# Kernel optimization log

Measured on AMD Instinct MI355X. Metric: run time of the kernel, lower is better.

Reference implementation:

```python
import jax, jax.numpy as jnp
import numpy as np

# Architecture constants (from init_kwargs)
IN_DIM, D_MODEL, HEADDIM, D_STATE, EXPAND, OUT_DIM = 57, 64, 32, 32, 2, 6
D_INNER = EXPAND * D_MODEL          # 128
NHEADS = D_INNER // HEADDIM         # 4
D_CONV = 4                          # causal depthwise conv width (mamba default)
D_XBC = D_INNER + 2 * D_STATE       # 192 (x, B, C share the conv)
D_IN_PROJ = 2 * D_INNER + 2 * D_STATE + NHEADS  # z, xBC, dt -> 324
BATCH, SEQ = 16, 2048


def setup_inputs() -> dict:
    key = jax.random.key(0)
    ks = jax.random.split(key, 12)
    s = 0.02
    return {
        "x": jax.random.normal(ks[0], (BATCH, SEQ, IN_DIM), jnp.float32),
        "W_lin": jax.random.normal(ks[1], (IN_DIM, D_MODEL), jnp.float32) * s,
        "b_lin": jnp.zeros((D_MODEL,), jnp.float32),
        "W_in": jax.random.normal(ks[2], (D_MODEL, D_IN_PROJ), jnp.float32) * s,
        "conv_w": jax.random.normal(ks[3], (D_XBC, 1, D_CONV), jnp.float32) * 0.5,
        "conv_b": jnp.zeros((D_XBC,), jnp.float32),
        "dt_bias": jnp.log(jax.random.uniform(ks[4], (NHEADS,), jnp.float32, 0.001, 0.1)),
        "A_log": jnp.log(jnp.arange(1, NHEADS + 1, dtype=jnp.float32)),
        "D": jnp.ones((NHEADS,), jnp.float32),
        "norm_w": jnp.ones((D_INNER,), jnp.float32),
        "W_out": jax.random.normal(ks[5], (D_INNER, D_MODEL), jnp.float32) * s,
        "W_cls": jax.random.normal(ks[6], (D_MODEL, OUT_DIM), jnp.float32) * s,
        "b_cls": jnp.zeros((OUT_DIM,), jnp.float32),
    }


def _mamba_block(h, W_in, conv_w, conv_b, dt_bias, A_log, D, norm_w, W_out):
    B, L, _ = h.shape
    zxbcdt = h @ W_in                                   # [B,L,324]
    z = zxbcdt[..., :D_INNER]                           # gate [B,L,128]
    xBC = zxbcdt[..., D_INNER:D_INNER + D_XBC]          # [B,L,192]
    dt = zxbcdt[..., D_INNER + D_XBC:]                  # [B,L,H]

    # causal depthwise conv over time + silu
    xBC = jax.lax.conv_general_dilated(
        xBC.transpose(0, 2, 1), conv_w, (1,), [(D_CONV - 1, 0)],
        dimension_numbers=("NCH", "OIH", "NCH"), feature_group_count=D_XBC)
    xBC = jax.nn.silu(xBC + conv_b[None, :, None]).transpose(0, 2, 1)

    xs = xBC[..., :D_INNER].reshape(B, L, NHEADS, HEADDIM)   # [B,L,H,P]
    Bm = xBC[..., D_INNER:D_INNER + D_STATE]                 # [B,L,N]
    Cm = xBC[..., D_INNER + D_STATE:]                        # [B,L,N]

    dt = jax.nn.softplus(dt + dt_bias)                       # [B,L,H]
    A = -jnp.exp(A_log)                                      # [H]

    def step(hstate, t):
        dtt, xt, bt, ct = t                                  # [B,H],[B,H,P],[B,N],[B,N]
        decay = jnp.exp(dtt * A)[:, :, None, None]           # [B,H,1,1]
        hstate = hstate * decay + (dtt[:, :, None] * xt)[..., None] * bt[:, None, None, :]
        y = jnp.einsum("bhpn,bn->bhp", hstate, ct)
        return hstate, y

    h0 = jnp.zeros((B, NHEADS, HEADDIM, D_STATE), h.dtype)
    _, ys = jax.lax.scan(step, h0, (dt.transpose(1, 0, 2), xs.transpose(1, 0, 2, 3),
                                    Bm.transpose(1, 0, 2), Cm.transpose(1, 0, 2)))
    y = ys.transpose(1, 0, 2, 3) + D[None, None, :, None] * xs   # [B,L,H,P]
    y = y.reshape(B, L, D_INNER)

    # gated RMSNorm + out proj
    y = y * jax.nn.silu(z)
    y = y * jax.lax.rsqrt(jnp.mean(y * y, axis=-1, keepdims=True) + 1e-5) * norm_w
    return y @ W_out                                        # [B,L,D_MODEL]


def reference(x, W_lin, b_lin, W_in, conv_w, conv_b, dt_bias, A_log, D, norm_w,
              W_out, W_cls, b_cls):
    h = x @ W_lin + b_lin                                   # linear_in
    h = _mamba_block(h, W_in, conv_w, conv_b, dt_bias, A_log, D, norm_w, W_out)
    pooled = h.mean(axis=1)                                 # AdaptiveAvgPool1d(1)
    return pooled @ W_cls + b_cls                           # classifier [B,6]
```

## Files before the change

### kernel.cpp

```cpp
#include <hip/hip_runtime.h>
#include <hip/hip_fp16.h>
#include <cmath>

#define BATCH   16
#define SEQ     2048
#define IN_DIM  57
#define D_MODEL 64
#define HEADDIM 32
#define D_STATE 32
#define OUT_DIM 6
#define D_INNER 128
#define NHEADS  4
#define D_CONV  4
#define D_XBC   192
#define D_XD    196
#define D_IN_PROJ 324
#define BL      (BATCH*SEQ)

#define NCHUNK  64
#define CLEN    (SEQ / NCHUNK)
#define SUBL    16

#define RTILE   24
#define XPAD    60

#define OFF_WF   ((size_t)0)
#define OFF_BF   ((size_t)18496)
#define OFF_WOC  ((size_t)18848)
#define OFF_G    ((size_t)19744)
#define OFF_P    ((size_t)21792)
#define OFF_DC   ((size_t)25920)
#define OFF_ZB   ((size_t)157000)
#define OFF_XD   (OFF_ZB + (size_t)BL*64)
#define OFF_CB   (OFF_XD + (size_t)BL*98)
#define OFF_YB   (OFF_CB + (size_t)BL*16)
#define OFF_SB   (OFF_YB + (size_t)BL*64)

__global__ void fuse_w_kernel(const float* __restrict__ W_lin,
                              const float* __restrict__ b_lin,
                              const float* __restrict__ W_in,
                              const float* __restrict__ W_out,
                              const float* __restrict__ W_cls,
                              float* __restrict__ Wf, float* __restrict__ bf,
                              float* __restrict__ Woc, float* __restrict__ G) {
    int idx = blockIdx.x * 256 + threadIdx.x;
    if (idx < BATCH * D_INNER) G[idx] = 0.f;
    if (idx < 58 * D_IN_PROJ) {
        int r = idx / D_IN_PROJ;
        int j = idx - r * D_IN_PROJ;
        const float* v = (r < IN_DIM) ? (W_lin + r * D_MODEL) : b_lin;
        float acc = 0.f;
#pragma unroll 8
        for (int m = 0; m < D_MODEL; ++m) acc += v[m] * W_in[m * D_IN_PROJ + j];
        if (r < IN_DIM) Wf[r * D_IN_PROJ + j] = acc;
        else            bf[j] = acc;
    } else if (idx < 58 * D_IN_PROJ + D_INNER * OUT_DIM) {
        int idx2 = idx - 58 * D_IN_PROJ;
        int i = idx2 / OUT_DIM;
        int o = idx2 - i * OUT_DIM;
        float acc = 0.f;
#pragma unroll 8
        for (int j = 0; j < D_MODEL; ++j)
            acc += W_out[i * D_MODEL + j] * W_cls[j * OUT_DIM + o];
        Woc[i * OUT_DIM + o] = acc;
    }
}

__global__ __launch_bounds__(256) void inproj_kernel(
        const float* __restrict__ x,
        const float* __restrict__ Wf,
        const float* __restrict__ bf,
        __half* __restrict__ zbh,
        __half* __restrict__ xdh) {
    __shared__ float xs[RTILE][XPAD];
    int r0 = blockIdx.x * RTILE;
    for (int i = threadIdx.x; i < RTILE * IN_DIM; i += 256) {
        size_t g = (size_t)r0 * IN_DIM + i;
        float v = (g < (size_t)BL * IN_DIM) ? x[g] : 0.f;
        xs[i / IN_DIM][i % IN_DIM] = v;
    }
    __syncthreads();
    if (threadIdx.x >= 243) return;
    int rset = threadIdx.x / 81;
    int cg   = threadIdx.x - rset * 81;
    int j0   = cg * 4;
    float4 bias = *(const float4*)(bf + j0);
    float4 acc[8];
#pragma unroll
    for (int r = 0; r < 8; ++r) acc[r] = bias;
    const float* w = Wf + j0;
    const float* xrow = &xs[rset * 8][0];
#pragma unroll 2
    for (int kc = 0; kc < 14; ++kc) {
        int k = kc * 4;
        float4 wv0 = *(const float4*)(w + (size_t)(k + 0) * D_IN_PROJ);
        float4 wv1 = *(const float4*)(w + (size_t)(k + 1) * D_IN_PROJ);
        float4 wv2 = *(const float4*)(w + (size_t)(k + 2) * D_IN_PROJ);
        float4 wv3 = *(const float4*)(w + (size_t)(k + 3) * D_IN_PROJ);
#pragma unroll
        for (int r = 0; r < 8; ++r) {
            float4 xv = *(const float4*)(xrow + r * XPAD + k);
            acc[r].x += xv.x * wv0.x + xv.y * wv1.x + xv.z * wv2.x + xv.w * wv3.x;
            acc[r].y += xv.x * wv0.y + xv.y * wv1.y + xv.z * wv2.y + xv.w * wv3.y;
            acc[r].z += xv.x * wv0.z + xv.y * wv1.z + xv.z * wv2.z + xv.w * wv3.z;
            acc[r].w += xv.x * wv0.w + xv.y * wv1.w + xv.z * wv2.w + xv.w * wv3.w;
        }
    }
    {
        float4 wv = *(const float4*)(w + (size_t)56 * D_IN_PROJ);
#pragma unroll
        for (int r = 0; r < 8; ++r) {
            float xv = xrow[r * XPAD + 56];
            acc[r].x += xv * wv.x; acc[r].y += xv * wv.y;
            acc[r].z += xv * wv.z; acc[r].w += xv * wv.w;
        }
    }
#pragma unroll
    for (int r = 0; r < 8; ++r) {
        int row = r0 + rset * 8 + r;
        if (row < BL) {
            __half2 h01 = __floats2half2_rn(acc[r].x, acc[r].y);
            __half2 h23 = __floats2half2_rn(acc[r].z, acc[r].w);
            uint2 u;
            u.x = *(unsigned*)&h01;
            u.y = *(unsigned*)&h23;
            if (j0 < D_INNER)
                *(uint2*)(zbh + (size_t)row * D_INNER + j0) = u;
            else
                *(uint2*)(xdh + (size_t)row * D_XD + (j0 - D_INNER)) = u;
        }
    }
}

__device__ __forceinline__ void conv_prologue(
        const __half* __restrict__ xdh,
        const float* __restrict__ conv_w, const float* __restrict__ conv_b,
        const float* __restrict__ dt_bias, const float* __restrict__ A_log,
        size_t rbase, int c, int tid,
        float (*xbt)[D_XBC], float (*ddl)[8]) {
    if (tid < D_XBC) {
        int ch = tid;
        float w0 = conv_w[ch*4+0], w1 = conv_w[ch*4+1];
        float w2 = conv_w[ch*4+2], w3 = conv_w[ch*4+3];
        float cb = conv_b[ch];
        const __half* src = xdh + rbase * D_XD + ch;
        float vm1 = 0.f, vm2 = 0.f, vm3 = 0.f;
        if (c > 0) {
            vm1 = __half2float(src[-(int)D_XD]);
            vm2 = __half2float(src[-2*(int)D_XD]);
            vm3 = __half2float(src[-3*(int)D_XD]);
        }
#pragma unroll
        for (int i = 0; i < CLEN; ++i) {
            float v0 = __half2float(src[(size_t)i * D_XD]);
            float a = cb + v0 * w3 + vm1 * w2 + vm2 * w1 + vm3 * w0;
            xbt[i][ch] = a / (1.f + expf(-a));
            vm3 = vm2; vm2 = vm1; vm1 = v0;
        }
    } else {
        int idx = tid - D_XBC;
        int h = idx >> 4;
        int i0 = idx & 15;
        float db = dt_bias[h];
        float nA = -expf(A_log[h]);
#pragma unroll
        for (int i = i0; i < CLEN; i += 16) {
            float v = __half2float(xdh[(rbase + i) * D_XD + 192 + h]) + db;
            float dtv = (v > 20.f) ? v : log1pf(expf(v));
            ddl[i][h * 2]     = dtv;
            ddl[i][h * 2 + 1] = expf(dtv * nA);
        }
    }
}

__global__ __launch_bounds__(256) void scan_phase1_kernel(
        const __half* __restrict__ xdh,
        const float* __restrict__ conv_w, const float* __restrict__ conv_b,
        const float* __restrict__ dt_bias, const float* __restrict__ A_log,
        const float* __restrict__ Dp,
        __half* __restrict__ sbuf, float* __restrict__ Pbuf,
        __half* __restrict__ ybuf, __half* __restrict__ Cbuf,
        float* __restrict__ Dcum) {
    int b = blockIdx.x >> 6;
    int c = blockIdx.x & (NCHUNK - 1);
    int tid = threadIdx.x;
    __shared__ float xbt[CLEN][D_XBC];
    __shared__ float ddl[CLEN][8];
    __shared__ __half yl[CLEN][D_INNER];
    __shared__ float dcl[CLEN * 4];
    size_t rbase = (size_t)b * SEQ + (size_t)c * CLEN;
    conv_prologue(xdh, conv_w, conv_b, dt_bias, A_log, rbase, c, tid, xbt, ddl);
    __syncthreads();
    int h = tid >> 6, lane = tid & 63;
    int p = lane >> 1, n0 = (lane & 1) * 16;
    float Dh = Dp[h];
    float4 s0 = make_float4(0.f,0.f,0.f,0.f), s1 = s0, s2 = s0, s3 = s0;
    float pacc = 1.f;
#pragma unroll 4
    for (int i = 0; i < CLEN; ++i) {
        float dtv = ddl[i][h * 2];
        float dec = ddl[i][h * 2 + 1];
        float xv = xbt[i][h * HEADDIM + p];
        const float* Bp = &xbt[i][D_INNER + n0];
        const float* Cp = &xbt[i][D_INNER + D_STATE + n0];
        float4 B0 = *(const float4*)(Bp + 0);
        float4 B1 = *(const float4*)(Bp + 4);
        float4 B2 = *(const float4*)(Bp + 8);
        float4 B3 = *(const float4*)(Bp + 12);
        float4 C0 = *(const float4*)(Cp + 0);
        float4 C1 = *(const float4*)(Cp + 4);
        float4 C2 = *(const float4*)(Cp + 8);
        float4 C3 = *(const float4*)(Cp + 12);
        float coef = dtv * xv;
        s0.x = s0.x*dec + coef*B0.x; s0.y = s0.y*dec + coef*B0.y;
        s0.z = s0.z*dec + coef*B0.z; s0.w = s0.w*dec + coef*B0.w;
        s1.x = s1.x*dec + coef*B1.x; s1.y = s1.y*dec + coef*B1.y;
        s1.z = s1.z*dec + coef*B1.z; s1.w = s1.w*dec + coef*B1.w;
        s2.x = s2.x*dec + coef*B2.x; s2.y = s2.y*dec + coef*B2.y;
        s2.z = s2.z*dec + coef*B2.z; s2.w = s2.w*dec + coef*B2.w;
        s3.x = s3.x*dec + coef*B3.x; s3.y = s3.y*dec + coef*B3.y;
        s3.z = s3.z*dec + coef*B3.z; s3.w = s3.w*dec + coef*B3.w;
        pacc *= dec;
        float part = s0.x*C0.x + s0.y*C0.y + s0.z*C0.z + s0.w*C0.w
                   + s1.x*C1.x + s1.y*C1.y + s1.z*C1.z + s1.w*C1.w
                   + s2.x*C2.x + s2.y*C2.y + s2.z*C2.z + s2.w*C2.w
                   + s3.x*C3.x + s3.y*C3.y + s3.z*C3.z + s3.w*C3.w;
        part += __shfl_xor(part, 1);
        if (lane == 0) dcl[i * 4 + h] = pacc;
        if ((lane & 1) == 0)
            yl[i][h * HEADDIM + p] = __float2half(part + Dh * xv);
    }
    int bh = b * NHEADS + h;
    __half2 hs[8];
    hs[0] = __floats2half2_rn(s0.x, s0.y); hs[1] = __floats2half2_rn(s0.z, s0.w);
    hs[2] = __floats2half2_rn(s1.x, s1.y); hs[3] = __floats2half2_rn(s1.z, s1.w);
    hs[4] = __floats2half2_rn(s2.x, s2.y); hs[5] = __floats2half2_rn(s2.z, s2.w);
    hs[6] = __floats2half2_rn(s3.x, s3.y); hs[7] = __floats2half2_rn(s3.z, s3.w);
    uint4* sp = (uint4*)(sbuf + ((size_t)bh * NCHUNK + c) * 1024) + lane * 2;
    sp[0] = *(uint4*)&hs[0];
    sp[1] = *(uint4*)&hs[4];
    if (lane == 0) Pbuf[bh * NCHUNK + c] = pacc;
    __syncthreads();
    {
        const uint4* ysrc = (const uint4*)&yl[0][0];
        uint4* ydst = (uint4*)(ybuf + rbase * D_INNER);
        ydst[tid]       = ysrc[tid];
        ydst[tid + 256] = ysrc[tid + 256];
    }
    for (int idx = tid; idx < CLEN * 16; idx += 256) {
        int r  = idx >> 4;
        int n2 = (idx & 15) * 2;
        __half2 hv = __floats2half2_rn(xbt[r][D_INNER + D_STATE + n2],
                                       xbt[r][D_INNER + D_STATE + n2 + 1]);
        *((__half2*)(Cbuf + (rbase + r) * D_STATE + n2)) = hv;
    }
    if (tid < CLEN * 4) Dcum[rbase * 4 + tid] = dcl[tid];
}

__global__ __launch_bounds__(256) void scan_phase2_kernel(
        __half* __restrict__ sbuf, const float* __restrict__ Pbuf) {
    __shared__ unsigned sl[NCHUNK][128];
    __shared__ float Pl[NCHUNK];
    int bh = blockIdx.x >> 2;
    int q  = blockIdx.x & 3;
    int tid = threadIdx.x;
    unsigned* s32 = (unsigned*)sbuf;
    size_t base = (size_t)bh * NCHUNK * 512 + (size_t)q * 128;
    if (tid < NCHUNK) Pl[tid] = Pbuf[bh * NCHUNK + tid];
    for (int k = tid; k < NCHUNK * 128; k += 256) {
        int c = k >> 7, j = k & 127;
        sl[c][j] = s32[base + (size_t)c * 512 + j];
    }
    __syncthreads();
    if (tid < 128) {
        float rx = 0.f, ry = 0.f;
        unsigned v = sl[0][tid];
#pragma unroll 8
        for (int c = 0; c < NCHUNK; ++c) {
            unsigned vn = (c + 1 < NCHUNK) ? sl[c + 1][tid] : 0u;
            float Pv = Pl[c];
            __half2 hv = *(__half2*)&v;
            float2 t = __half22float2(hv);
            __half2 hr = __floats2half2_rn(rx, ry);
            sl[c][tid] = *(unsigned*)&hr;
            rx = rx * Pv + t.x;
            ry = ry * Pv + t.y;
            v = vn;
        }
    }
    __syncthreads();
    for (int k = tid; k < NCHUNK * 128; k += 256) {
        int c = k >> 7, j = k & 127;
        s32[base + (size_t)c * 512 + j] = sl[c][j];
    }
}

__global__ __launch_bounds__(256) void scan_phase3_kernel(
        const __half* __restrict__ ybuf, const __half* __restrict__ Cbuf,
        const float* __restrict__ Dcum, const __half* __restrict__ zbh,
        const __half* __restrict__ sbuf, const float* __restrict__ norm_w,
        float* __restrict__ G) {
    int b  = blockIdx.x >> 7;
    int sc = blockIdx.x & 127;
    int c  = sc >> 1;
    int tid = threadIdx.x;
    __shared__ float ylds[SUBL][D_INNER];
    __shared__ float dcl[SUBL * 4];
    __shared__ float red[4][D_INNER];
    size_t rbase = (size_t)b * SEQ + (size_t)sc * SUBL;
    int h = tid >> 6, lane = tid & 63;
    int p = lane >> 1, n0 = (lane & 1) * 16;
    int bh = b * NHEADS + h;
    const uint4* sp = (const uint4*)(sbuf + ((size_t)bh * NCHUNK + c) * 1024) + lane * 2;
    uint4 u0 = sp[0], u1 = sp[1];
    {
        const __half2* ysrc = (const __half2*)(ybuf + rbase * D_INNER);
#pragma unroll
        for (int k = 0; k < 4; ++k) {
            int idx = tid + k * 256;
            float2 f = __half22float2(ysrc[idx]);
            int r  = idx >> 6;
            int c2 = (idx & 63) * 2;
            ylds[r][c2]     = f.x;
            ylds[r][c2 + 1] = f.y;
        }
    }
    if (tid < SUBL * 4) dcl[tid] = Dcum[rbase * 4 + tid];
    float4 s0, s1, s2, s3;
    {
        const __half2* hp0 = (const __half2*)&u0;
        const __half2* hp1 = (const __half2*)&u1;
        float2 f;
        f = __half22float2(hp0[0]); s0.x = f.x; s0.y = f.y;
        f = __half22float2(hp0[1]); s0.z = f.x; s0.w = f.y;
        f = __half22float2(hp0[2]); s1.x = f.x; s1.y = f.y;
        f = __half22float2(hp0[3]); s1.z = f.x; s1.w = f.y;
        f = __half22float2(hp1[0]); s2.x = f.x; s2.y = f.y;
        f = __half22float2(hp1[1]); s2.z = f.x; s2.w = f.y;
        f = __half22float2(hp1[2]); s3.x = f.x; s3.y = f.y;
        f = __half22float2(hp1[3]); s3.z = f.x; s3.w = f.y;
    }
    __syncthreads();
#pragma unroll 4
    for (int i = 0; i < SUBL; ++i) {
        const uint4* cp = (const uint4*)(Cbuf + (rbase + i) * D_STATE + n0);
        uint4 ca = cp[0], cb = cp[1];
        const __half2* cha = (const __half2*)&ca;
        const __half2* chb = (const __half2*)&cb;
        float2 f0 = __half22float2(cha[0]);
        float2 f1 = __half22float2(cha[1]);
        float2 f2 = __half22float2(cha[2]);
        float2 f3 = __half22float2(cha[3]);
        float2 f4 = __half22float2(chb[0]);
        float2 f5 = __half22float2(chb[1]);
        float2 f6 = __half22float2(chb[2]);
        float2 f7 = __half22float2(chb[3]);
        float part = s0.x*f0.x + s0.y*f0.y + s0.z*f1.x + s0.w*f1.y
                   + s1.x*f2.x + s1.y*f2.y + s1.z*f3.x + s1.w*f3.y
                   + s2.x*f4.x + s2.y*f4.y + s2.z*f5.x + s2.w*f5.y
                   + s3.x*f6.x + s3.y*f6.y + s3.z*f7.x + s3.w*f7.y;
        part += __shfl_xor(part, 1);
        if ((lane & 1) == 0)
            ylds[i][h * HEADDIM + p] += dcl[i * 4 + h] * part;
    }
    __syncthreads();
    float acc0 = 0.f, acc1 = 0.f;
    for (int r = h; r < SUBL; r += 4) {
        size_t bl = rbase + r;
        float2 yv = *(const float2*)(&ylds[r][lane * 2]);
        float2 zv = __half22float2(*((const __half2*)(zbh + bl * D_INNER) + lane));
        float g0 = yv.x * (zv.x / (1.f + expf(-zv.x)));
        float g1 = yv.y * (zv.y / (1.f + expf(-zv.y)));
        float sq = g0 * g0 + g1 * g1;
#pragma unroll
        for (int m = 1; m < 64; m <<= 1) sq += __shfl_xor(sq, m);
        float rms = 1.0f / sqrtf(sq * (1.f / 128.f) + 1e-5f);
        acc0 += g0 * rms;
        acc1 += g1 * rms;
    }
    red[h][lane * 2]     = acc0;
    red[h][lane * 2 + 1] = acc1;
    __syncthreads();
    if (tid < D_INNER) {
        float sg = red[0][tid] + red[1][tid] + red[2][tid] + red[3][tid];
        atomicAdd(&G[b * D_INNER + tid], sg * norm_w[tid]);
    }
}

__global__ void head_kernel(const float* __restrict__ G,
                            const float* __restrict__ Woc,
                            const float* __restrict__ b_cls,
                            float* __restrict__ out) {
    int tid = threadIdx.x;
    if (tid >= BATCH * OUT_DIM) return;
    int b = tid / OUT_DIM, o = tid - b * OUT_DIM;
    float acc = 0.f;
#pragma unroll 8
    for (int i = 0; i < D_INNER; ++i)
        acc += G[b * D_INNER + i] * Woc[i * OUT_DIM + o];
    out[b * OUT_DIM + o] = acc * (1.f / (float)SEQ) + b_cls[o];
}

extern "C" void kernel_launch(void* const* d_in, const int* in_sizes, int n_in,
                              void* d_out, int out_size, void* d_ws, size_t ws_size,
                              hipStream_t stream) {
    const float* x       = (const float*)d_in[0];
    const float* W_lin   = (const float*)d_in[1];
    const float* b_lin   = (const float*)d_in[2];
    const float* W_in    = (const float*)d_in[3];
    const float* conv_w  = (const float*)d_in[4];
    const float* conv_b  = (const float*)d_in[5];
    const float* dt_bias = (const float*)d_in[6];
    const float* A_log   = (const float*)d_in[7];
    const float* Dp      = (const float*)d_in[8];
    const float* norm_w  = (const float*)d_in[9];
    const float* W_out   = (const float*)d_in[10];
    const float* W_cls   = (const float*)d_in[11];
    const float* b_cls   = (const float*)d_in[12];
    float* out = (float*)d_out;

    float* ws = (float*)d_ws;
    float* Wf    = ws + OFF_WF;
    float* bf    = ws + OFF_BF;
    float* Woc   = ws + OFF_WOC;
    float* G     = ws + OFF_G;
    float* Pbuf  = ws + OFF_P;
    float* Dcum  = ws + OFF_DC;
    __half* zbh  = (__half*)(ws + OFF_ZB);
    __half* xdh  = (__half*)(ws + OFF_XD);
    __half* Cbh  = (__half*)(ws + OFF_CB);
    __half* ybh  = (__half*)(ws + OFF_YB);
    __half* sbuf = (__half*)(ws + OFF_SB);

    fuse_w_kernel<<<(58 * D_IN_PROJ + D_INNER * OUT_DIM + 255) / 256, 256, 0, stream>>>(
        W_lin, b_lin, W_in, W_out, W_cls, Wf, bf, Woc, G);

    inproj_kernel<<<(BL + RTILE - 1) / RTILE, 256, 0, stream>>>(x, Wf, bf, zbh, xdh);

    scan_phase1_kernel<<<BATCH * NCHUNK, 256, 0, stream>>>(
        xdh, conv_w, conv_b, dt_bias, A_log, Dp, sbuf, Pbuf, ybh, Cbh, Dcum);
    scan_phase2_kernel<<<256, 256, 0, stream>>>(sbuf, Pbuf);
    scan_phase3_kernel<<<BATCH * 128, 256, 0, stream>>>(
        ybh, Cbh, Dcum, zbh, sbuf, norm_w, G);

    head_kernel<<<1, 128, 0, stream>>>(G, Woc, b_cls, out);
}
```

Before: 170.4 us.

## Fuse input projection into scan phase 1 and fold classifier head into phase 3

The input projection is merged into the chunked scan's first phase. Each block recomputes the x/B/C/dt projection for its 32-row chunk plus a 3-row conv halo in shared memory, so the fp16 xBC/dt intermediate is never written to or read back from global memory. The classifier head is folded into phase 3: each block multiplies its pooled partial by the fused out/classifier weights and atomically adds into the output, which is pre-initialised with the bias. This removes two kernel launches and a large intermediate buffer, at the cost of redundant halo projection work and more float atomics on the output.

Measured after the change: 168.1 us. About the same (-1.3%).

```diff
diff --git a/kernel.cpp b/kernel.cpp
--- a/kernel.cpp
+++ b/kernel.cpp
@@ -13,26 +13,21 @@
 #define NHEADS  4
 #define D_CONV  4
 #define D_XBC   192
-#define D_XD    196
 #define D_IN_PROJ 324
 #define BL      (BATCH*SEQ)
 
 #define NCHUNK  64
 #define CLEN    (SEQ / NCHUNK)
 #define SUBL    16
-
-#define RTILE   24
-#define XPAD    60
+#define XDS     200
 
 #define OFF_WF   ((size_t)0)
 #define OFF_BF   ((size_t)18496)
 #define OFF_WOC  ((size_t)18848)
-#define OFF_G    ((size_t)19744)
 #define OFF_P    ((size_t)21792)
 #define OFF_DC   ((size_t)25920)
 #define OFF_ZB   ((size_t)157000)
-#define OFF_XD   (OFF_ZB + (size_t)BL*64)
-#define OFF_CB   (OFF_XD + (size_t)BL*98)
+#define OFF_CB   (OFF_ZB + (size_t)BL*64)
 #define OFF_YB   (OFF_CB + (size_t)BL*16)
 #define OFF_SB   (OFF_YB + (size_t)BL*64)
 
@@ -42,9 +37,11 @@
                               const float* __restrict__ W_out,
                               const float* __restrict__ W_cls,
                               float* __restrict__ Wf, float* __restrict__ bf,
-                              float* __restrict__ Woc, float* __restrict__ G) {
+                              float* __restrict__ Woc,
+                              const float* __restrict__ b_cls,
+                              float* __restrict__ out) {
     int idx = blockIdx.x * 256 + threadIdx.x;
-    if (idx < BATCH * D_INNER) G[idx] = 0.f;
+    if (idx < BATCH * OUT_DIM) out[idx] = b_cls[idx % OUT_DIM];
     if (idx < 58 * D_IN_PROJ) {
         int r = idx / D_IN_PROJ;
         int j = idx - r * D_IN_PROJ;
@@ -66,93 +63,140 @@
     }
 }
 
-__global__ __launch_bounds__(256) void inproj_kernel(
+__global__ __launch_bounds__(256) void mega1_kernel(
         const float* __restrict__ x,
-        const float* __restrict__ Wf,
-        const float* __restrict__ bf,
+        const float* __restrict__ Wf, const float* __restrict__ bf,
+        const float* __restrict__ conv_w, const float* __restrict__ conv_b,
+        const float* __restrict__ dt_bias, const float* __restrict__ A_log,
+        const float* __restrict__ Dp,
         __half* __restrict__ zbh,
-        __half* __restrict__ xdh) {
-    __shared__ float xs[RTILE][XPAD];
-    int r0 = blockIdx.x * RTILE;
-    for (int i = threadIdx.x; i < RTILE * IN_DIM; i += 256) {
-        size_t g = (size_t)r0 * IN_DIM + i;
-        float v = (g < (size_t)BL * IN_DIM) ? x[g] : 0.f;
-        xs[i / IN_DIM][i % IN_DIM] = v;
-    }
-    __syncthreads();
-    if (threadIdx.x >= 243) return;
-    int rset = threadIdx.x / 81;
-    int cg   = threadIdx.x - rset * 81;
-    int j0   = cg * 4;
-    float4 bias = *(const float4*)(bf + j0);
-    float4 acc[8];
-#pragma unroll
-    for (int r = 0; r < 8; ++r) acc[r] = bias;
-    const float* w = Wf + j0;
-    const float* xrow = &xs[rset * 8][0];
+        __half* __restrict__ sbuf, float* __restrict__ Pbuf,
+        __half* __restrict__ ybuf, __half* __restrict__ Cbuf,
+        float* __restrict__ Dcum) {
+    __shared__ __align__(16) char smem[40112];
+    float (*xs)[60]    = (float (*)[60])smem;
+    float (*xbt)[D_XBC]= (float (*)[D_XBC])smem;
+    __half (*xdl)[XDS] = (__half (*)[XDS])(smem + 24576);
+    __half (*yl)[D_INNER] = (__half (*)[D_INNER])(smem + 24576);
+    float (*ddl)[8]    = (float (*)[8])(smem + 38576);
+    float* dcl         = (float*)(smem + 39600);
+
+    int b = blockIdx.x >> 6;
+    int c = blockIdx.x & (NCHUNK - 1);
+    int tid = threadIdx.x;
+    long rbase = (long)b * SEQ + (long)c * CLEN;
+
+    for (int i = tid; i < 35 * IN_DIM; i += 256) {
+        int r = i / IN_DIM, k = i - r * IN_DIM;
+        float v = 0.f;
+        if (c > 0 || r >= 3) v = x[(rbase - 3 + r) * IN_DIM + k];
+        xs[r][k] = v;
+    }
+    __syncthreads();
+
+    if (tid < 245) {
+        int rset = tid / 49, cg = tid - rset * 49;
+        int j0 = 128 + cg * 4;
+        float4 bias = *(const float4*)(bf + j0);
+        float4 acc[7];
+#pragma unroll
+        for (int r = 0; r < 7; ++r) acc[r] = bias;
+        const float* w = Wf + j0;
+        const float* xrow = &xs[rset * 7][0];
 #pragma unroll 2
-    for (int kc = 0; kc < 14; ++kc) {
-        int k = kc * 4;
-        float4 wv0 = *(const float4*)(w + (size_t)(k + 0) * D_IN_PROJ);
-        float4 wv1 = *(const float4*)(w + (size_t)(k + 1) * D_IN_PROJ);
-        float4 wv2 = *(const float4*)(w + (size_t)(k + 2) * D_IN_PROJ);
-        float4 wv3 = *(const float4*)(w + (size_t)(k + 3) * D_IN_PROJ);
-#pragma unroll
-        for (int r = 0; r < 8; ++r) {
-            float4 xv = *(const float4*)(xrow + r * XPAD + k);
-            acc[r].x += xv.x * wv0.x + xv.y * wv1.x + xv.z * wv2.x + xv.w * wv3.x;
-            acc[r].y += xv.x * wv0.y + xv.y * wv1.y + xv.z * wv2.y + xv.w * wv3.y;
-            acc[r].z += xv.x * wv0.z + xv.y * wv1.z + xv.z * wv2.z + xv.w * wv3.z;
-            acc[r].w += xv.x * wv0.w + xv.y * wv1.w + xv.z * wv2.w + xv.w * wv3.w;
-        }
-    }
+        for (int kc = 0; kc < 14; ++kc) {
+            int k = kc * 4;
+            float4 wv0 = *(const float4*)(w + (size_t)(k + 0) * D_IN_PROJ);
+            float4 wv1 = *(const float4*)(w + (size_t)(k + 1) * D_IN_PROJ);
+            float4 wv2 = *(const float4*)(w + (size_t)(k + 2) * D_IN_PROJ);
+            float4 wv3 = *(const float4*)(w + (size_t)(k + 3) * D_IN_PROJ);
+#pragma unroll
+            for (int r = 0; r < 7; ++r) {
+                float4 xv = *(const float4*)(xrow + r * 60 + k);
+                acc[r].x += xv.x * wv0.x + xv.y * wv1.x + xv.z * wv2.x + xv.w * wv3.x;
+                acc[r].y += xv.x * wv0.y + xv.y * wv1.y + xv.z * wv2.y + xv.w * wv3.y;
+                acc[r].z += xv.x * wv0.z + xv.y * wv1.z + xv.z * wv2.z + xv.w * wv3.z;
+                acc[r].w += xv.x * wv0.w + xv.y * wv1.w + xv.z * wv2.w + xv.w * wv3.w;
+            }
+        }
+        {
+            float4 wv = *(const float4*)(w + (size_t)56 * D_IN_PROJ);
+#pragma unroll
+            for (int r = 0; r < 7; ++r) {
+                float xv = xrow[r * 60 + 56];
+                acc[r].x += xv * wv.x; acc[r].y += xv * wv.y;
+                acc[r].z += xv * wv.z; acc[r].w += xv * wv.w;
+            }
+        }
+#pragma unroll
+        for (int r = 0; r < 7; ++r) {
+            int row = rset * 7 + r;
+            *(__half2*)&xdl[row][j0 - 128]     = __floats2half2_rn(acc[r].x, acc[r].y);
+            *(__half2*)&xdl[row][j0 - 128 + 2] = __floats2half2_rn(acc[r].z, acc[r].w);
+        }
+    }
+
     {
-        float4 wv = *(const float4*)(w + (size_t)56 * D_IN_PROJ);
-#pragma unroll
-        for (int r = 0; r < 8; ++r) {
-            float xv = xrow[r * XPAD + 56];
-            acc[r].x += xv * wv.x; acc[r].y += xv * wv.y;
-            acc[r].z += xv * wv.z; acc[r].w += xv * wv.w;
-        }
-    }
-#pragma unroll
-    for (int r = 0; r < 8; ++r) {
-        int row = r0 + rset * 8 + r;
-        if (row < BL) {
+        int rset = tid >> 5, cg = tid & 31;
+        int j0 = cg * 4;
+        float4 bias = *(const float4*)(bf + j0);
+        float4 acc[4];
+#pragma unroll
+        for (int r = 0; r < 4; ++r) acc[r] = bias;
+        const float* w = Wf + j0;
+        const float* xrow = &xs[3 + rset * 4][0];
+#pragma unroll 2
+        for (int kc = 0; kc < 14; ++kc) {
+            int k = kc * 4;
+            float4 wv0 = *(const float4*)(w + (size_t)(k + 0) * D_IN_PROJ);
+            float4 wv1 = *(const float4*)(w + (size_t)(k + 1) * D_IN_PROJ);
+            float4 wv2 = *(const float4*)(w + (size_t)(k + 2) * D_IN_PROJ);
+            float4 wv3 = *(const float4*)(w + (size_t)(k + 3) * D_IN_PROJ);
+#pragma unroll
+            for (int r = 0; r < 4; ++r) {
+                float4 xv = *(const float4*)(xrow + r * 60 + k);
+                acc[r].x += xv.x * wv0.x + xv.y * wv1.x + xv.z * wv2.x + xv.w * wv3.x;
+                acc[r].y += xv.x * wv0.y + xv.y * wv1.y + xv.z * wv2.y + xv.w * wv3.y;
+                acc[r].z += xv.x * wv0.z + xv.y * wv1.z + xv.z * wv2.z + xv.w * wv3.z;
+                acc[r].w += xv.x * wv0.w + xv.y * wv1.w + xv.z * wv2.w + xv.w * wv3.w;
+            }
+        }
+        {
+            float4 wv = *(const float4*)(w + (size_t)56 * D_IN_PROJ);
+#pragma unroll
+            for (int r = 0; r < 4; ++r) {
+                float xv = xrow[r * 60 + 56];
+                acc[r].x += xv * wv.x; acc[r].y += xv * wv.y;
+                acc[r].z += xv * wv.z; acc[r].w += xv * wv.w;
+            }
+        }
+#pragma unroll
+        for (int r = 0; r < 4; ++r) {
+            long row = rbase + rset * 4 + r;
             __half2 h01 = __floats2half2_rn(acc[r].x, acc[r].y);
             __half2 h23 = __floats2half2_rn(acc[r].z, acc[r].w);
             uint2 u;
             u.x = *(unsigned*)&h01;
             u.y = *(unsigned*)&h23;
-            if (j0 < D_INNER)
-                *(uint2*)(zbh + (size_t)row * D_INNER + j0) = u;
-            else
-                *(uint2*)(xdh + (size_t)row * D_XD + (j0 - D_INNER)) = u;
-        }
-    }
-}
-
-__device__ __forceinline__ void conv_prologue(
-        const __half* __restrict__ xdh,
-        const float* __restrict__ conv_w, const float* __restrict__ conv_b,
-        const float* __restrict__ dt_bias, const float* __restrict__ A_log,
-        size_t rbase, int c, int tid,
-        float (*xbt)[D_XBC], float (*ddl)[8]) {
+            *(uint2*)(zbh + row * D_INNER + j0) = u;
+        }
+    }
+    __syncthreads();
+
     if (tid < D_XBC) {
         int ch = tid;
         float w0 = conv_w[ch*4+0], w1 = conv_w[ch*4+1];
         float w2 = conv_w[ch*4+2], w3 = conv_w[ch*4+3];
         float cb = conv_b[ch];
-        const __half* src = xdh + rbase * D_XD + ch;
         float vm1 = 0.f, vm2 = 0.f, vm3 = 0.f;
         if (c > 0) {
-            vm1 = __half2float(src[-(int)D_XD]);
-            vm2 = __half2float(src[-2*(int)D_XD]);
-            vm3 = __half2float(src[-3*(int)D_XD]);
+            vm1 = __half2float(xdl[2][ch]);
+            vm2 = __half2float(xdl[1][ch]);
+            vm3 = __half2float(xdl[0][ch]);
         }
 #pragma unroll
         for (int i = 0; i < CLEN; ++i) {
-            float v0 = __half2float(src[(size_t)i * D_XD]);
+            float v0 = __half2float(xdl[i + 3][ch]);
             float a = cb + v0 * w3 + vm1 * w2 + vm2 * w1 + vm3 * w0;
             xbt[i][ch] = a / (1.f + expf(-a));
             vm3 = vm2; vm2 = vm1; vm1 = v0;
@@ -165,32 +209,14 @@
         float nA = -expf(A_log[h]);
 #pragma unroll
         for (int i = i0; i < CLEN; i += 16) {
-            float v = __half2float(xdh[(rbase + i) * D_XD + 192 + h]) + db;
+            float v = __half2float(xdl[i + 3][192 + h]) + db;
             float dtv = (v > 20.f) ? v : log1pf(expf(v));
             ddl[i][h * 2]     = dtv;
             ddl[i][h * 2 + 1] = expf(dtv * nA);
         }
     }
-}
-
-__global__ __launch_bounds__(256) void scan_phase1_kernel(
-        const __half* __restrict__ xdh,
-        const float* __restrict__ conv_w, const float* __restrict__ conv_b,
-        const float* __restrict__ dt_bias, const float* __restrict__ A_log,
-        const float* __restrict__ Dp,
-        __half* __restrict__ sbuf, float* __restrict__ Pbuf,
-        __half* __restrict__ ybuf, __half* __restrict__ Cbuf,
-        float* __restrict__ Dcum) {
-    int b = blockIdx.x >> 6;
-    int c = blockIdx.x & (NCHUNK - 1);
-    int tid = threadIdx.x;
-    __shared__ float xbt[CLEN][D_XBC];
-    __shared__ float ddl[CLEN][8];
-    __shared__ __half yl[CLEN][D_INNER];
-    __shared__ float dcl[CLEN * 4];
-    size_t rbase = (size_t)b * SEQ + (size_t)c * CLEN;
-    conv_prologue(xdh, conv_w, conv_b, dt_bias, A_log, rbase, c, tid, xbt, ddl);
-    __syncthreads();
+    __syncthreads();
+
     int h = tid >> 6, lane = tid & 63;
     int p = lane >> 1, n0 = (lane & 1) * 16;
     float Dh = Dp[h];
@@ -243,7 +269,7 @@
     __syncthreads();
     {
         const uint4* ysrc = (const uint4*)&yl[0][0];
-        uint4* ydst = (uint4*)(ybuf + rbase * D_INNER);
+        uint4* ydst = (uint4*)(ybuf + (size_t)rbase * D_INNER);
         ydst[tid]       = ysrc[tid];
         ydst[tid + 256] = ysrc[tid + 256];
     }
@@ -252,9 +278,9 @@
         int n2 = (idx & 15) * 2;
         __half2 hv = __floats2half2_rn(xbt[r][D_INNER + D_STATE + n2],
                                        xbt[r][D_INNER + D_STATE + n2 + 1]);
-        *((__half2*)(Cbuf + (rbase + r) * D_STATE + n2)) = hv;
-    }
-    if (tid < CLEN * 4) Dcum[rbase * 4 + tid] = dcl[tid];
+        *((__half2*)(Cbuf + ((size_t)rbase + r) * D_STATE + n2)) = hv;
+    }
+    if (tid < CLEN * 4) Dcum[(size_t)rbase * 4 + tid] = dcl[tid];
 }
 
 __global__ __launch_bounds__(256) void scan_phase2_kernel(
@@ -299,7 +325,7 @@
         const __half* __restrict__ ybuf, const __half* __restrict__ Cbuf,
         const float* __restrict__ Dcum, const __half* __restrict__ zbh,
         const __half* __restrict__ sbuf, const float* __restrict__ norm_w,
-        float* __restrict__ G) {
+        const float* __restrict__ Woc, float* __restrict__ out) {
     int b  = blockIdx.x >> 7;
     int sc = blockIdx.x & 127;
     int c  = sc >> 1;
@@ -307,6 +333,7 @@
     __shared__ float ylds[SUBL][D_INNER];
     __shared__ float dcl[SUBL * 4];
     __shared__ float red[4][D_INNER];
+    __shared__ float snw[D_INNER];
     size_t rbase = (size_t)b * SEQ + (size_t)sc * SUBL;
     int h = tid >> 6, lane = tid & 63;
     int p = lane >> 1, n0 = (lane & 1) * 16;
@@ -381,24 +408,17 @@
     red[h][lane * 2]     = acc0;
     red[h][lane * 2 + 1] = acc1;
     __syncthreads();
-    if (tid < D_INNER) {
-        float sg = red[0][tid] + red[1][tid] + red[2][tid] + red[3][tid];
-        atomicAdd(&G[b * D_INNER + tid], sg * norm_w[tid]);
-    }
-}
-
-__global__ void head_kernel(const float* __restrict__ G,
-                            const float* __restrict__ Woc,
-                            const float* __restrict__ b_cls,
-                            float* __restrict__ out) {
-    int tid = threadIdx.x;
-    if (tid >= BATCH * OUT_DIM) return;
-    int b = tid / OUT_DIM, o = tid - b * OUT_DIM;
-    float acc = 0.f;
+    if (tid < D_INNER)
+        snw[tid] = (red[0][tid] + red[1][tid] + red[2][tid] + red[3][tid])
+                   * norm_w[tid];
+    __syncthreads();
+    if (tid < OUT_DIM) {
+        float acc = 0.f;
 #pragma unroll 8
-    for (int i = 0; i < D_INNER; ++i)
-        acc += G[b * D_INNER + i] * Woc[i * OUT_DIM + o];
-    out[b * OUT_DIM + o] = acc * (1.f / (float)SEQ) + b_cls[o];
+        for (int i = 0; i < D_INNER; ++i)
+            acc += snw[i] * Woc[i * OUT_DIM + tid];
+        atomicAdd(&out[b * OUT_DIM + tid], acc * (1.f / (float)SEQ));
+    }
 }
 
 extern "C" void kernel_launch(void* const* d_in, const int* in_sizes, int n_in,
@@ -423,25 +443,22 @@
     float* Wf    = ws + OFF_WF;
     float* bf    = ws + OFF_BF;
     float* Woc   = ws + OFF_WOC;
-    float* G     = ws + OFF_G;
     float* Pbuf  = ws + OFF_P;
     float* Dcum  = ws + OFF_DC;
     __half* zbh  = (__half*)(ws + OFF_ZB);
-    __half* xdh  = (__half*)(ws + OFF_XD);
     __half* Cbh  = (__half*)(ws + OFF_CB);
     __half* ybh  = (__half*)(ws + OFF_YB);
     __half* sbuf = (__half*)(ws + OFF_SB);
 
     fuse_w_kernel<<<(58 * D_IN_PROJ + D_INNER * OUT_DIM + 255) / 256, 256, 0, stream>>>(
-        W_lin, b_lin, W_in, W_out, W_cls, Wf, bf, Woc, G);
-
-    inproj_kernel<<<(BL + RTILE - 1) / RTILE, 256, 0, stream>>>(x, Wf, bf, zbh, xdh);
-
-    scan_phase1_kernel<<<BATCH * NCHUNK, 256, 0, stream>>>(
-        xdh, conv_w, conv_b, dt_bias, A_log, Dp, sbuf, Pbuf, ybh, Cbh, Dcum);
+        W_lin, b_lin, W_in, W_out, W_cls, Wf, bf, Woc, b_cls, out);
+
+    mega1_kernel<<<BATCH * NCHUNK, 256, 0, stream>>>(
+        x, Wf, bf, conv_w, conv_b, dt_bias, A_log, Dp,
+        zbh, sbuf, Pbuf, ybh, Cbh, Dcum);
+
     scan_phase2_kernel<<<256, 256, 0, stream>>>(sbuf, Pbuf);
+
     scan_phase3_kernel<<<BATCH * 128, 256, 0, stream>>>(
-        ybh, Cbh, Dcum, zbh, sbuf, norm_w, G);
-
-    head_kernel<<<1, 128, 0, stream>>>(G, Woc, b_cls, out);
+        ybh, Cbh, Dcum, zbh, sbuf, norm_w, Woc, out);
 }
```
